# Performance work log

Measured on AMD Instinct MI355X. Metric: run time of the kernel, lower is better.

Reference implementation:

```python
import jax, jax.numpy as jnp
import numpy as np

B, S, E, H = 2, 4096, 768, 12
D = E // H  # head_dim = 64
SCALE = D ** -0.5
NEG = -1e9


def setup_inputs() -> dict:
    key = jax.random.key(0)
    ks = jax.random.split(key, 10)
    init = lambda k, shape: jax.random.normal(k, shape, dtype=jnp.float32) * (shape[-1] ** -0.5)
    x = jax.random.normal(ks[0], (B, S, E), dtype=jnp.float32)
    attention_mask = jnp.zeros((B, 1, S, S), dtype=jnp.float32)
    # additive causal mask: 0 on/below diagonal, -1e9 above
    causal = jnp.where(jnp.tril(jnp.ones((S, S), dtype=bool)), 0.0, NEG).astype(jnp.float32)
    causal_attention_mask = causal[None, None]
    return {
        "x": x,
        "attention_mask": attention_mask,
        "causal_attention_mask": causal_attention_mask,
        "Wq": init(ks[1], (E, E)), "bq": jnp.zeros((E,), jnp.float32),
        "Wk": init(ks[2], (E, E)), "bk": jnp.zeros((E,), jnp.float32),
        "Wv": init(ks[3], (E, E)), "bv": jnp.zeros((E,), jnp.float32),
        "Wo": init(ks[4], (E, E)), "bo": jnp.zeros((E,), jnp.float32),
    }


def _split_heads(t):
    # [B,S,E] -> [B,H,S,D]
    return t.reshape(B, S, H, D).transpose(0, 2, 1, 3)


def reference(x, attention_mask, causal_attention_mask, Wq, bq, Wk, bk, Wv, bv, Wo, bo):
    q = _split_heads(x @ Wq.T + bq)
    k = _split_heads(x @ Wk.T + bk)
    v = _split_heads(x @ Wv.T + bv)
    mask = attention_mask + causal_attention_mask  # [B,1,S,S]
    scores = jnp.einsum("bhqd,bhkd->bhqk", q, k) * SCALE + mask
    probs = jax.nn.softmax(scores.astype(jnp.float32), axis=-1).astype(q.dtype)
    out = jnp.einsum("bhqk,bhkd->bhqd", probs, v)
    out = out.transpose(0, 2, 1, 3).reshape(B, S, E)
    return out @ Wo.T + bo
```

## Files before the change

### kernel.cpp

```cpp
#include <hip/hip_runtime.h>
#include <hip/hip_bf16.h>
#include <stdint.h>

#define B_ 2
#define S_ 4096
#define E_ 768
#define H_ 12
#define D_ 64
#define M_TOT (B_*S_)
#define NQKV (3*E_)

typedef __attribute__((ext_vector_type(8)))  short bf16x8;
typedef __attribute__((ext_vector_type(4)))  float f32x4;
typedef __attribute__((ext_vector_type(16))) float f32x16;
typedef unsigned short u16;
typedef unsigned int   u32;

__device__ __forceinline__ u16 f2bf(float f) {
  __hip_bfloat16 h = __float2bfloat16(f);
  return *reinterpret_cast<u16*>(&h);
}

__device__ __forceinline__ u32 cvtpk(float lo, float hi) {
  u32 r;
  asm("v_cvt_pk_bf16_f32 %0, %1, %2" : "=v"(r) : "v"(lo), "v"(hi));
  return r;
}

#define GLDS(gp, lp) __builtin_amdgcn_global_load_lds( \
    (const __attribute__((address_space(1))) void*)(gp), \
    (__attribute__((address_space(3))) void*)(lp), 16, 0, 0)


__global__ void k_cast_x(const float* __restrict__ x, u16* __restrict__ xb) {
  int i = blockIdx.x * blockDim.x + threadIdx.x;
  float4 v = reinterpret_cast<const float4*>(x)[i];
  ushort4 o;
  o.x = f2bf(v.x); o.y = f2bf(v.y); o.z = f2bf(v.z); o.w = f2bf(v.w);
  reinterpret_cast<ushort4*>(xb)[i] = o;
}

#define QSCALE 0.1803368801111573f

__global__ void k_pack_wqkv(const float* __restrict__ Wq, const float* __restrict__ Wk,
                            const float* __restrict__ Wv, const float* __restrict__ bq,
                            const float* __restrict__ bk, const float* __restrict__ bv,
                            u16* __restrict__ wqkv, float* __restrict__ bqkv) {
  int i = blockIdx.x * blockDim.x + threadIdx.x;
  int base = i * 4;
  int n = base / E_;
  int k = base % E_;
  const float* src; float sc;
  if (n < E_)        { src = Wq + (size_t)n*E_ + k;          sc = QSCALE; }
  else if (n < 2*E_) { src = Wk + (size_t)(n-E_)*E_ + k;     sc = 1.f; }
  else               { src = Wv + (size_t)(n-2*E_)*E_ + k;   sc = 1.f; }
  float4 v = *reinterpret_cast<const float4*>(src);
  ushort4 o;
  o.x = f2bf(v.x*sc); o.y = f2bf(v.y*sc); o.z = f2bf(v.z*sc); o.w = f2bf(v.w*sc);
  reinterpret_cast<ushort4*>(wqkv)[i] = o;
  if (i < NQKV) {
    float b = (i < E_) ? bq[i]*QSCALE : (i < 2*E_) ? bk[i-E_] : bv[i-2*E_];
    bqkv[i] = b;
  }
}

__global__ void k_cast_wo(const float* __restrict__ Wo, u16* __restrict__ wo) {
  int i = blockIdx.x * blockDim.x + threadIdx.x;
  float4 v = reinterpret_cast<const float4*>(Wo)[i];
  ushort4 o;
  o.x = f2bf(v.x); o.y = f2bf(v.y); o.z = f2bf(v.z); o.w = f2bf(v.w);
  reinterpret_cast<ushort4*>(wo)[i] = o;
}


template<int MODE>
__global__ __launch_bounds__(256)
void k_gemm(const u16* __restrict__ A, const u16* __restrict__ W,
            const float* __restrict__ bias,
            u16* __restrict__ dq, u16* __restrict__ dk, u16* __restrict__ dv,
            float* __restrict__ fout)
{
  __shared__ u16 As[128*64];
  __shared__ u16 Ws[128*64];
  const int tid  = threadIdx.x;
  const int lane = tid & 63, wave = tid >> 6;
  const int m0 = blockIdx.x * 128;
  const int n0 = blockIdx.y * 128;
  const int g  = lane >> 4, cc = lane & 15;
  const int wr = (wave >> 1) * 64, wc = (wave & 1) * 64;
  const int srow = lane >> 3;
  const int scol = (lane & 7) * 8;

  f32x4 acc[4][4];
  #pragma unroll
  for (int m = 0; m < 4; ++m)
    #pragma unroll
    for (int n = 0; n < 4; ++n) acc[m][n] = (f32x4){0.f,0.f,0.f,0.f};

  for (int k0 = 0; k0 < E_; k0 += 64) {
    __syncthreads();
    #pragma unroll
    for (int i = 0; i < 4; ++i) {
      const int r0 = (i*4 + wave) * 8;
      GLDS(A + (size_t)(m0 + r0 + srow)*E_ + k0 + scol, As + r0*64);
      GLDS(W + (size_t)(n0 + r0 + srow)*E_ + k0 + scol, Ws + r0*64);
    }
    __syncthreads();
    #pragma unroll
    for (int kk = 0; kk < 64; kk += 32) {
      bf16x8 af[4], bfr[4];
      #pragma unroll
      for (int m = 0; m < 4; ++m)
        af[m] = *reinterpret_cast<const bf16x8*>(As + (wr + m*16 + cc)*64 + kk + g*8);
      #pragma unroll
      for (int n = 0; n < 4; ++n)
        bfr[n] = *reinterpret_cast<const bf16x8*>(Ws + (wc + n*16 + cc)*64 + kk + g*8);
      #pragma unroll
      for (int m = 0; m < 4; ++m)
        #pragma unroll
        for (int n = 0; n < 4; ++n)
          acc[m][n] = __builtin_amdgcn_mfma_f32_16x16x32_bf16(af[m], bfr[n], acc[m][n], 0, 0, 0);
    }
  }

  #pragma unroll
  for (int n = 0; n < 4; ++n) {
    const int colg = n0 + wc + n*16 + cc;
    const float bb = bias[colg];
    if (MODE == 0) {
      const int which = colg / E_;
      const int nn = colg % E_;
      const int h = nn >> 6, d = nn & 63;
      #pragma unroll
      for (int m = 0; m < 4; ++m)
        #pragma unroll
        for (int j = 0; j < 4; ++j) {
          const int row = m0 + wr + m*16 + g*4 + j;
          const int b = row >> 12, s = row & (S_-1);
          const u16 val = f2bf(acc[m][n][j] + bb);
          if (which == 0)       dq[(((size_t)b*H_ + h)*S_ + s)*D_ + d] = val;
          else if (which == 1)  dk[(((size_t)b*H_ + h)*S_ + s)*D_ + d] = val;
          else                  dv[(((size_t)b*H_ + h)*D_ + d)*S_ + s] = val;
        }
    } else {
      #pragma unroll
      for (int m = 0; m < 4; ++m)
        #pragma unroll
        for (int j = 0; j < 4; ++j) {
          const int row = m0 + wr + m*16 + g*4 + j;
          fout[(size_t)row*E_ + colg] = acc[m][n][j] + bb;
        }
    }
  }
}


__global__ __launch_bounds__(256, 3)
void k_attn(const u16* __restrict__ Qb, const u16* __restrict__ Kb,
            const u16* __restrict__ Vtg, u16* __restrict__ AO)
{
  __shared__ u16 Ks[2][32*128];
  __shared__ u16 Vs[2][32*128];
  const int tid = threadIdx.x, lane = tid & 63, w = tid >> 6;

  const int L  = blockIdx.x;
  const int kk = L >> 8;
  const int j  = L & 255;
  const int x  = j & 7;
  const int c  = j >> 3;
  const int bh = x*3 + kk;
  const int u  = c >> 1;
  int qt;
  if (kk == 0)      qt = c;
  else if (kk == 1) qt = (c & 1) ? ((u < 15) ? 14 - u : 15) : 31 - u;
  else              qt = (c & 1) ? ((u < 15) ? 31 - u : 0)  : 16 - u;

  const int q0 = qt * 128;
  const int ntiles = 2*qt + 2;

  const size_t kbase = (size_t)bh * S_ * D_;
  const size_t vbase = (size_t)bh * D_ * S_;
  const int hi = lane >> 5, l31 = lane & 31;
  const int swz = (lane & 15) << 4;
  const int qg = q0 + w*32 + l31;

  int stA[2], stB[2];
  #pragma unroll
  for (int i = 0; i < 2; ++i) {
    const int jj = 2*w + i;
    const int row = jj*4 + (lane >> 4);
    const int gb = ((lane & 15) * 16) ^ ((row & 15) << 4);
    stA[i] = row + 32*(gb >> 7);
    stB[i] = (gb & 127) >> 1;
  }

  bf16x8 qf[4];
  #pragma unroll
  for (int ds = 0; ds < 4; ++ds)
    qf[ds] = *reinterpret_cast<const bf16x8*>(Qb + kbase + (size_t)qg*D_ + ds*16 + hi*8);

  float m_run = -INFINITY, l_run = 0.f;
  f32x16 o0, o1;
  #pragma unroll
  for (int r = 0; r < 16; ++r) { o0[r] = 0.f; o1[r] = 0.f; }

#define STAGE(buf, kv0_) do { \
    _Pragma("unroll") \
    for (int i = 0; i < 2; ++i) { \
      GLDS(Kb  + kbase + (size_t)((kv0_) + stA[i])*D_ + stB[i], &Ks[buf][(2*w+i)*512]); \
      GLDS(Vtg + vbase + (size_t)stA[i]*S_ + (kv0_) + stB[i],   &Vs[buf][(2*w+i)*512]); \
    } } while(0)

  int cur = 0;
  STAGE(0, 0);

  for (int t = 0; t < ntiles; ++t) {
    const int kv0 = t * 64;
    asm volatile("s_waitcnt vmcnt(0)" ::: "memory");
    __builtin_amdgcn_s_barrier();
    asm volatile("" ::: "memory");
    if (t + 1 < ntiles) STAGE(cur ^ 1, (t+1)*64);

    const u16* bK = Ks[cur];
    const u16* bV = Vs[cur];

    f32x16 s0, s1;
    #pragma unroll
    for (int r = 0; r < 16; ++r) { s0[r] = 0.f; s1[r] = 0.f; }
    __builtin_amdgcn_s_setprio(1);
    #pragma unroll
    for (int ds = 0; ds < 4; ++ds) {
      const int off = ((32*ds + 16*hi) ^ swz) >> 1;
      bf16x8 a0 = *reinterpret_cast<const bf16x8*>(bK + l31*128 + off);
      bf16x8 a1 = *reinterpret_cast<const bf16x8*>(bK + l31*128 + (off ^ 64));
      s0 = __builtin_amdgcn_mfma_f32_32x32x16_bf16(a0, qf[ds], s0, 0, 0, 0);
      s1 = __builtin_amdgcn_mfma_f32_32x32x16_bf16(a1, qf[ds], s1, 0, 0, 0);
    }
    __builtin_amdgcn_s_setprio(0);

    if (t >= ntiles - 2) {
      #pragma unroll
      for (int r = 0; r < 16; ++r) {
        const int kvl = kv0 + (r&3) + 8*(r>>2) + 4*hi;
        s0[r] = (kvl      > qg) ? -1e30f : s0[r];
        s1[r] = (kvl + 32 > qg) ? -1e30f : s1[r];
      }
    }

    float m4[8];
    #pragma unroll
    for (int i = 0; i < 4; ++i)
      m4[i] = fmaxf(fmaxf(s0[4*i], s0[4*i+1]), fmaxf(s0[4*i+2], s0[4*i+3]));
    #pragma unroll
    for (int i = 0; i < 4; ++i)
      m4[4+i] = fmaxf(fmaxf(s1[4*i], s1[4*i+1]), fmaxf(s1[4*i+2], s1[4*i+3]));
    float mx = fmaxf(fmaxf(fmaxf(m4[0], m4[1]), fmaxf(m4[2], m4[3])),
                     fmaxf(fmaxf(m4[4], m4[5]), fmaxf(m4[6], m4[7])));
    mx = fmaxf(mx, __shfl_xor(mx, 32));

    if (!__all(mx <= m_run + 8.0f)) {
      const float mnew  = fmaxf(m_run, mx);
      const float alpha = exp2f(m_run - mnew);
      m_run = mnew;
      l_run *= alpha;
      #pragma unroll
      for (int r = 0; r < 16; ++r) { o0[r] *= alpha; o1[r] *= alpha; }
    }

    #pragma unroll
    for (int r = 0; r < 16; ++r) s0[r] = exp2f(s0[r] - m_run);
    #pragma unroll
    for (int r = 0; r < 16; ++r) s1[r] = exp2f(s1[r] - m_run);
    float t4[8];
    #pragma unroll
    for (int i = 0; i < 4; ++i)
      t4[i] = (s0[4*i] + s0[4*i+1]) + (s0[4*i+2] + s0[4*i+3]);
    #pragma unroll
    for (int i = 0; i < 4; ++i)
      t4[4+i] = (s1[4*i] + s1[4*i+1]) + (s1[4*i+2] + s1[4*i+3]);
    float sum = ((t4[0]+t4[1]) + (t4[2]+t4[3])) + ((t4[4]+t4[5]) + (t4[6]+t4[7]));
    sum += __shfl_xor(sum, 32);
    l_run += sum;

    u32 c16[16];
    #pragma unroll
    for (int i = 0; i < 8; ++i) {
      c16[i]   = cvtpk(s0[2*i], s0[2*i+1]);
      c16[8+i] = cvtpk(s1[2*i], s1[2*i+1]);
    }

    #pragma unroll
    for (int ks = 0; ks < 4; ++ks) {
      const int cb = (ks>>1)*8 + (ks&1)*4;
      u32 x0 = c16[cb],   y0 = c16[cb+2];
      u32 x1 = c16[cb+1], y1 = c16[cb+3];
      asm volatile("v_permlane32_swap_b32 %0, %1" : "+v"(x0), "+v"(y0));
      asm volatile("v_permlane32_swap_b32 %0, %1" : "+v"(x1), "+v"(y1));
      union { u32 u[4]; bf16x8 v; } pf;
      pf.u[0] = x0; pf.u[1] = x1; pf.u[2] = y0; pf.u[3] = y1;
      const int voff = ((32*ks + 16*hi) ^ swz) >> 1;
      bf16x8 v0 = *reinterpret_cast<const bf16x8*>(bV + l31*128 + voff);
      bf16x8 v1 = *reinterpret_cast<const bf16x8*>(bV + l31*128 + (voff ^ 64));
      __builtin_amdgcn_s_setprio(1);
      o0 = __builtin_amdgcn_mfma_f32_32x32x16_bf16(v0, pf.v, o0, 0, 0, 0);
      o1 = __builtin_amdgcn_mfma_f32_32x32x16_bf16(v1, pf.v, o1, 0, 0, 0);
      __builtin_amdgcn_s_setprio(0);
    }

    asm volatile("" ::: "memory");
    __builtin_amdgcn_s_barrier();
    cur ^= 1;
  }
#undef STAGE

  const int b = bh / H_, h = bh % H_;
  const float inv = 1.0f / l_run;
  u16* dst = AO + ((size_t)b*S_ + qg)*E_ + h*64;
  #pragma unroll
  for (int aa = 0; aa < 4; ++aa) {
    ushort4 wv;
    wv.x = f2bf(o0[4*aa+0]*inv); wv.y = f2bf(o0[4*aa+1]*inv);
    wv.z = f2bf(o0[4*aa+2]*inv); wv.w = f2bf(o0[4*aa+3]*inv);
    *reinterpret_cast<ushort4*>(dst + aa*8 + hi*4) = wv;
  }
  #pragma unroll
  for (int aa = 0; aa < 4; ++aa) {
    ushort4 wv;
    wv.x = f2bf(o1[4*aa+0]*inv); wv.y = f2bf(o1[4*aa+1]*inv);
    wv.z = f2bf(o1[4*aa+2]*inv); wv.w = f2bf(o1[4*aa+3]*inv);
    *reinterpret_cast<ushort4*>(dst + 32 + aa*8 + hi*4) = wv;
  }
}


extern "C" void kernel_launch(void* const* d_in, const int* in_sizes, int n_in,
                              void* d_out, int out_size, void* d_ws, size_t ws_size,
                              hipStream_t stream) {
  const float* x  = (const float*)d_in[0];
  const float* Wq = (const float*)d_in[3];
  const float* bq = (const float*)d_in[4];
  const float* Wk = (const float*)d_in[5];
  const float* bk = (const float*)d_in[6];
  const float* Wv = (const float*)d_in[7];
  const float* bv = (const float*)d_in[8];
  const float* Wo = (const float*)d_in[9];
  const float* bo = (const float*)d_in[10];
  float* out = (float*)d_out;

  const size_t SZ_X   = (size_t)M_TOT * E_ * 2;
  const size_t SZ_WQKV= (size_t)NQKV * E_ * 2;
  const size_t SZ_WO  = (size_t)E_ * E_ * 2;
  const size_t SZ_B   = (size_t)NQKV * 4;
  char* w = (char*)d_ws;
  u16*   xb   = (u16*)(w);
  u16*   wqkv = (u16*)(w + SZ_X);
  u16*   wob  = (u16*)(w + SZ_X + SZ_WQKV);
  float* bqkv = (float*)(w + SZ_X + SZ_WQKV + SZ_WO);
  char*  w2   = w + SZ_X + SZ_WQKV + SZ_WO + SZ_B;
  u16* Qb = (u16*)(w2);
  u16* Kb = (u16*)(w2 + SZ_X);
  u16* Vb = (u16*)(w2 + 2*SZ_X);
  u16* AO = (u16*)(w2 + 3*SZ_X);

  k_cast_x  <<<6144, 256, 0, stream>>>(x, xb);
  k_pack_wqkv<<<1728, 256, 0, stream>>>(Wq, Wk, Wv, bq, bk, bv, wqkv, bqkv);
  k_cast_wo <<<576,  256, 0, stream>>>(Wo, wob);

  dim3 gq(64, 18);
  k_gemm<0><<<gq, 256, 0, stream>>>(xb, wqkv, bqkv, Qb, Kb, Vb, nullptr);

  k_attn<<<768, 256, 0, stream>>>(Qb, Kb, Vb, AO);

  dim3 go(64, 6);
  k_gemm<1><<<go, 256, 0, stream>>>(AO, wob, bo, nullptr, nullptr, nullptr, out);
}
```

Before: 233.6 us.

## Split long causal attention rows across two blocks and merge with combine kernel

The attention kernel now splits the KV range of the longer query tiles (qt>=16) into two partial blocks. Each block writes unnormalized bf16 partial outputs plus its running max and sum, and a new k_comb kernel merges the two halves. This is meant to balance work across CUs and shorten the critical path. The block-to-work schedule is rebuilt for 1152 blocks and occupancy is raised to 5 per CU. Diagonal tiles are processed first so the running max starts from real values, the max reduction uses v_max3, and rescaling is folded into the score init. The costs are an extra launch, the partial-result traffic through a reused workspace buffer, and one more bf16 rounding of the partials.

New measurement: 285.6 us. 1.22x slower.

```diff
diff --git a/kernel.cpp b/kernel.cpp
--- a/kernel.cpp
+++ b/kernel.cpp
@@ -21,15 +21,27 @@
   return *reinterpret_cast<u16*>(&h);
 }
 
+__device__ __forceinline__ float bf2f(u16 u) {
+  union { u32 i; float f; } v; v.i = ((u32)u) << 16; return v.f;
+}
+
 __device__ __forceinline__ u32 cvtpk(float lo, float hi) {
   u32 r;
   asm("v_cvt_pk_bf16_f32 %0, %1, %2" : "=v"(r) : "v"(lo), "v"(hi));
   return r;
 }
 
+__device__ __forceinline__ float max3f(float a, float b, float c) {
+  float d;
+  asm("v_max3_f32 %0, %1, %2, %3" : "=v"(d) : "v"(a), "v"(b), "v"(c));
+  return d;
+}
+
 #define GLDS(gp, lp) __builtin_amdgcn_global_load_lds( \
     (const __attribute__((address_space(1))) void*)(gp), \
     (__attribute__((address_space(3))) void*)(lp), 16, 0, 0)
+
+#define QSCALE 0.1803368801111573f
 
 
 __global__ void k_cast_x(const float* __restrict__ x, u16* __restrict__ xb) {
@@ -39,8 +51,6 @@
   o.x = f2bf(v.x); o.y = f2bf(v.y); o.z = f2bf(v.z); o.w = f2bf(v.w);
   reinterpret_cast<ushort4*>(xb)[i] = o;
 }
-
-#define QSCALE 0.1803368801111573f
 
 __global__ void k_pack_wqkv(const float* __restrict__ Wq, const float* __restrict__ Wk,
                             const float* __restrict__ Wv, const float* __restrict__ bq,
@@ -51,9 +61,9 @@
   int n = base / E_;
   int k = base % E_;
   const float* src; float sc;
-  if (n < E_)        { src = Wq + (size_t)n*E_ + k;          sc = QSCALE; }
-  else if (n < 2*E_) { src = Wk + (size_t)(n-E_)*E_ + k;     sc = 1.f; }
-  else               { src = Wv + (size_t)(n-2*E_)*E_ + k;   sc = 1.f; }
+  if (n < E_)        { src = Wq + (size_t)n*E_ + k;        sc = QSCALE; }
+  else if (n < 2*E_) { src = Wk + (size_t)(n-E_)*E_ + k;   sc = 1.f; }
+  else               { src = Wv + (size_t)(n-2*E_)*E_ + k; sc = 1.f; }
   float4 v = *reinterpret_cast<const float4*>(src);
   ushort4 o;
   o.x = f2bf(v.x*sc); o.y = f2bf(v.y*sc); o.z = f2bf(v.z*sc); o.w = f2bf(v.w*sc);
@@ -155,34 +165,44 @@
 }
 
 
-__global__ __launch_bounds__(256, 3)
+__global__ __launch_bounds__(256, 5)
 void k_attn(const u16* __restrict__ Qb, const u16* __restrict__ Kb,
-            const u16* __restrict__ Vtg, u16* __restrict__ AO)
+            const u16* __restrict__ Vtg, u16* __restrict__ AO,
+            u16* __restrict__ PO, float2* __restrict__ PML)
 {
   __shared__ u16 Ks[2][32*128];
   __shared__ u16 Vs[2][32*128];
   const int tid = threadIdx.x, lane = tid & 63, w = tid >> 6;
 
-  const int L  = blockIdx.x;
-  const int kk = L >> 8;
-  const int j  = L & 255;
-  const int x  = j & 7;
-  const int c  = j >> 3;
-  const int bh = x*3 + kk;
-  const int u  = c >> 1;
-  int qt;
-  if (kk == 0)      qt = c;
-  else if (kk == 1) qt = (c & 1) ? ((u < 15) ? 14 - u : 15) : 31 - u;
-  else              qt = (c & 1) ? ((u < 15) ? 31 - u : 0)  : 16 - u;
-
+  const int L    = blockIdx.x;
+  const int slot = L >> 8;
+  const int cu   = L & 255;
+  const int x    = cu & 7;
+  const int c    = cu >> 3;
+  int r;
+  if (slot < 4) r = slot*32 + ((slot & 1) ? (31 - c) : c);
+  else          r = 128 + c;
+  int head, qt, mode;
+  if (r < 120) {
+    const int g_ = r / 15, o = r % 15;
+    if (o < 9) {
+      if (o < 3) { head = o; qt = 15 - g_; mode = 0; }
+      else { const int hh = o - 3; head = hh >> 1; mode = 1 + (hh & 1); qt = 31 - 2*g_; }
+    } else { const int hh = o - 9; head = hh >> 1; mode = 1 + (hh & 1); qt = 30 - 2*g_; }
+  } else {
+    const int rr = r - 120; qt = 7 - rr/3; head = rr % 3; mode = 0;
+  }
+  const int bh = x*3 + head;
   const int q0 = qt * 128;
-  const int ntiles = 2*qt + 2;
+  const int nt = (mode == 0) ? (2*qt + 2) : (qt + 1);
 
   const size_t kbase = (size_t)bh * S_ * D_;
   const size_t vbase = (size_t)bh * D_ * S_;
   const int hi = lane >> 5, l31 = lane & 31;
   const int swz = (lane & 15) << 4;
   const int qg = q0 + w*32 + l31;
+
+  #define KVT(it_) ((mode == 1) ? (it_) : ((it_) == 0 ? 2*qt : ((it_) == 1 ? 2*qt+1 : ((mode == 0) ? (it_) - 2 : qt + (it_) - 1))))
 
   int stA[2], stB[2];
   #pragma unroll
@@ -199,10 +219,10 @@
   for (int ds = 0; ds < 4; ++ds)
     qf[ds] = *reinterpret_cast<const bf16x8*>(Qb + kbase + (size_t)qg*D_ + ds*16 + hi*8);
 
-  float m_run = -INFINITY, l_run = 0.f;
+  float m_run = 0.f, l_run = 0.f;
   f32x16 o0, o1;
   #pragma unroll
-  for (int r = 0; r < 16; ++r) { o0[r] = 0.f; o1[r] = 0.f; }
+  for (int r2 = 0; r2 < 16; ++r2) { o0[r2] = 0.f; o1[r2] = 0.f; }
 
 #define STAGE(buf, kv0_) do { \
     _Pragma("unroll") \
@@ -212,21 +232,22 @@
     } } while(0)
 
   int cur = 0;
-  STAGE(0, 0);
-
-  for (int t = 0; t < ntiles; ++t) {
-    const int kv0 = t * 64;
+  STAGE(0, KVT(0)*64);
+
+  for (int it = 0; it < nt; ++it) {
     asm volatile("s_waitcnt vmcnt(0)" ::: "memory");
     __builtin_amdgcn_s_barrier();
     asm volatile("" ::: "memory");
-    if (t + 1 < ntiles) STAGE(cur ^ 1, (t+1)*64);
-
+    if (it + 1 < nt) STAGE(cur ^ 1, KVT(it+1)*64);
+
+    const int kv0 = KVT(it) * 64;
     const u16* bK = Ks[cur];
     const u16* bV = Vs[cur];
 
+    const float minit = (it == 0) ? 0.f : -m_run;
     f32x16 s0, s1;
     #pragma unroll
-    for (int r = 0; r < 16; ++r) { s0[r] = 0.f; s1[r] = 0.f; }
+    for (int r2 = 0; r2 < 16; ++r2) { s0[r2] = minit; s1[r2] = minit; }
     __builtin_amdgcn_s_setprio(1);
     #pragma unroll
     for (int ds = 0; ds < 4; ++ds) {
@@ -238,39 +259,52 @@
     }
     __builtin_amdgcn_s_setprio(0);
 
-    if (t >= ntiles - 2) {
-      #pragma unroll
-      for (int r = 0; r < 16; ++r) {
-        const int kvl = kv0 + (r&3) + 8*(r>>2) + 4*hi;
-        s0[r] = (kvl      > qg) ? -1e30f : s0[r];
-        s1[r] = (kvl + 32 > qg) ? -1e30f : s1[r];
+    if (mode != 1 && it <= 1) {
+      #pragma unroll
+      for (int r2 = 0; r2 < 16; ++r2) {
+        const int kvl = kv0 + (r2&3) + 8*(r2>>2) + 4*hi;
+        s0[r2] = (kvl      > qg) ? -1e30f : s0[r2];
+        s1[r2] = (kvl + 32 > qg) ? -1e30f : s1[r2];
       }
     }
 
-    float m4[8];
-    #pragma unroll
-    for (int i = 0; i < 4; ++i)
-      m4[i] = fmaxf(fmaxf(s0[4*i], s0[4*i+1]), fmaxf(s0[4*i+2], s0[4*i+3]));
-    #pragma unroll
-    for (int i = 0; i < 4; ++i)
-      m4[4+i] = fmaxf(fmaxf(s1[4*i], s1[4*i+1]), fmaxf(s1[4*i+2], s1[4*i+3]));
-    float mx = fmaxf(fmaxf(fmaxf(m4[0], m4[1]), fmaxf(m4[2], m4[3])),
-                     fmaxf(fmaxf(m4[4], m4[5]), fmaxf(m4[6], m4[7])));
+    float a0_ = max3f(s0[0],  s0[1],  s0[2]);
+    float a1_ = max3f(s0[3],  s0[4],  s0[5]);
+    float a2_ = max3f(s0[6],  s0[7],  s0[8]);
+    float a3_ = max3f(s0[9],  s0[10], s0[11]);
+    float a4_ = max3f(s0[12], s0[13], s0[14]);
+    float a5_ = max3f(s1[0],  s1[1],  s1[2]);
+    float a6_ = max3f(s1[3],  s1[4],  s1[5]);
+    float a7_ = max3f(s1[6],  s1[7],  s1[8]);
+    float a8_ = max3f(s1[9],  s1[10], s1[11]);
+    float a9_ = max3f(s1[12], s1[13], s1[14]);
+    float b0_ = max3f(a0_, a1_, a2_);
+    float b1_ = max3f(a3_, a4_, s0[15]);
+    float b2_ = max3f(a5_, a6_, a7_);
+    float b3_ = max3f(a8_, a9_, s1[15]);
+    float mx  = max3f(b0_, b1_, fmaxf(b2_, b3_));
     mx = fmaxf(mx, __shfl_xor(mx, 32));
 
-    if (!__all(mx <= m_run + 8.0f)) {
-      const float mnew  = fmaxf(m_run, mx);
-      const float alpha = exp2f(m_run - mnew);
-      m_run = mnew;
+    if (it == 0) {
+      m_run = mx;
+      #pragma unroll
+      for (int r2 = 0; r2 < 16; ++r2) { s0[r2] -= mx; s1[r2] -= mx; }
+    } else if (!__all(mx <= 24.0f)) {
+      const float mxc   = fmaxf(mx, 0.f);
+      const float alpha = exp2f(-mxc);
+      m_run += mxc;
       l_run *= alpha;
       #pragma unroll
-      for (int r = 0; r < 16; ++r) { o0[r] *= alpha; o1[r] *= alpha; }
-    }
-
-    #pragma unroll
-    for (int r = 0; r < 16; ++r) s0[r] = exp2f(s0[r] - m_run);
-    #pragma unroll
-    for (int r = 0; r < 16; ++r) s1[r] = exp2f(s1[r] - m_run);
+      for (int r2 = 0; r2 < 16; ++r2) {
+        o0[r2] *= alpha; o1[r2] *= alpha;
+        s0[r2] -= mxc;   s1[r2] -= mxc;
+      }
+    }
+    #pragma unroll
+    for (int r2 = 0; r2 < 16; ++r2) s0[r2] = exp2f(s0[r2]);
+    #pragma unroll
+    for (int r2 = 0; r2 < 16; ++r2) s1[r2] = exp2f(s1[r2]);
+
     float t4[8];
     #pragma unroll
     for (int i = 0; i < 4; ++i)
@@ -312,23 +346,87 @@
     cur ^= 1;
   }
 #undef STAGE
-
+#undef KVT
+
+  if (mode == 0) {
+    const int b = bh / H_, h = bh % H_;
+    const float inv = 1.0f / l_run;
+    u16* dst = AO + ((size_t)b*S_ + qg)*E_ + h*64;
+    #pragma unroll
+    for (int aa = 0; aa < 4; ++aa) {
+      ushort4 wv;
+      wv.x = f2bf(o0[4*aa+0]*inv); wv.y = f2bf(o0[4*aa+1]*inv);
+      wv.z = f2bf(o0[4*aa+2]*inv); wv.w = f2bf(o0[4*aa+3]*inv);
+      *reinterpret_cast<ushort4*>(dst + aa*8 + hi*4) = wv;
+    }
+    #pragma unroll
+    for (int aa = 0; aa < 4; ++aa) {
+      ushort4 wv;
+      wv.x = f2bf(o1[4*aa+0]*inv); wv.y = f2bf(o1[4*aa+1]*inv);
+      wv.z = f2bf(o1[4*aa+2]*inv); wv.w = f2bf(o1[4*aa+3]*inv);
+      *reinterpret_cast<ushort4*>(dst + 32 + aa*8 + hi*4) = wv;
+    }
+  } else {
+    const int qslot = (bh*16 + (qt-16))*2 + (mode - 1);
+    const int rowt = w*32 + l31;
+    u16* po = PO + (size_t)qslot*(128*64) + rowt*64;
+    #pragma unroll
+    for (int aa = 0; aa < 4; ++aa) {
+      ushort4 wv;
+      wv.x = f2bf(o0[4*aa+0]); wv.y = f2bf(o0[4*aa+1]);
+      wv.z = f2bf(o0[4*aa+2]); wv.w = f2bf(o0[4*aa+3]);
+      *reinterpret_cast<ushort4*>(po + aa*8 + hi*4) = wv;
+    }
+    #pragma unroll
+    for (int aa = 0; aa < 4; ++aa) {
+      ushort4 wv;
+      wv.x = f2bf(o1[4*aa+0]); wv.y = f2bf(o1[4*aa+1]);
+      wv.z = f2bf(o1[4*aa+2]); wv.w = f2bf(o1[4*aa+3]);
+      *reinterpret_cast<ushort4*>(po + 32 + aa*8 + hi*4) = wv;
+    }
+    if (hi == 0) PML[qslot*128 + rowt] = make_float2(m_run, l_run);
+  }
+}
+
+
+__global__ __launch_bounds__(256)
+void k_comb(const u16* __restrict__ PO, const float2* __restrict__ PML,
+            u16* __restrict__ AO)
+{
+  const int bid = blockIdx.x;
+  const int bh = bid >> 4, qi = bid & 15, q = 16 + qi;
+  const int t = threadIdx.x;
+  const int r = t >> 1, half = t & 1;
+  const int s0 = (bh*16 + qi)*2, s1 = s0 + 1;
+  const float2 ml0 = PML[s0*128 + r];
+  const float2 ml1 = PML[s1*128 + r];
+  const float mstar = fmaxf(ml0.x, ml1.x);
+  const float w0 = exp2f(ml0.x - mstar);
+  const float w1 = exp2f(ml1.x - mstar);
+  const float inv = 1.0f / (ml0.y*w0 + ml1.y*w1);
+  const float a0 = w0 * inv, a1 = w1 * inv;
+  const u16* p0 = PO + (size_t)s0*(128*64) + r*64 + half*32;
+  const u16* p1 = PO + (size_t)s1*(128*64) + r*64 + half*32;
   const int b = bh / H_, h = bh % H_;
-  const float inv = 1.0f / l_run;
-  u16* dst = AO + ((size_t)b*S_ + qg)*E_ + h*64;
-  #pragma unroll
-  for (int aa = 0; aa < 4; ++aa) {
-    ushort4 wv;
-    wv.x = f2bf(o0[4*aa+0]*inv); wv.y = f2bf(o0[4*aa+1]*inv);
-    wv.z = f2bf(o0[4*aa+2]*inv); wv.w = f2bf(o0[4*aa+3]*inv);
-    *reinterpret_cast<ushort4*>(dst + aa*8 + hi*4) = wv;
-  }
-  #pragma unroll
-  for (int aa = 0; aa < 4; ++aa) {
-    ushort4 wv;
-    wv.x = f2bf(o1[4*aa+0]*inv); wv.y = f2bf(o1[4*aa+1]*inv);
-    wv.z = f2bf(o1[4*aa+2]*inv); wv.w = f2bf(o1[4*aa+3]*inv);
-    *reinterpret_cast<ushort4*>(dst + 32 + aa*8 + hi*4) = wv;
+  const int row = q*128 + r;
+  u16* dst = AO + ((size_t)b*S_ + row)*E_ + h*64 + half*32;
+  #pragma unroll
+  for (int i = 0; i < 4; ++i) {
+    bf16x8 v0 = *reinterpret_cast<const bf16x8*>(p0 + i*8);
+    bf16x8 v1 = *reinterpret_cast<const bf16x8*>(p1 + i*8);
+    ushort4 lo, hi4;
+    float f0 = bf2f(((const u16*)&v0)[0])*a0 + bf2f(((const u16*)&v1)[0])*a1;
+    float f1 = bf2f(((const u16*)&v0)[1])*a0 + bf2f(((const u16*)&v1)[1])*a1;
+    float f2 = bf2f(((const u16*)&v0)[2])*a0 + bf2f(((const u16*)&v1)[2])*a1;
+    float f3 = bf2f(((const u16*)&v0)[3])*a0 + bf2f(((const u16*)&v1)[3])*a1;
+    lo.x = f2bf(f0); lo.y = f2bf(f1); lo.z = f2bf(f2); lo.w = f2bf(f3);
+    float f4 = bf2f(((const u16*)&v0)[4])*a0 + bf2f(((const u16*)&v1)[4])*a1;
+    float f5 = bf2f(((const u16*)&v0)[5])*a0 + bf2f(((const u16*)&v1)[5])*a1;
+    float f6 = bf2f(((const u16*)&v0)[6])*a0 + bf2f(((const u16*)&v1)[6])*a1;
+    float f7 = bf2f(((const u16*)&v0)[7])*a0 + bf2f(((const u16*)&v1)[7])*a1;
+    hi4.x = f2bf(f4); hi4.y = f2bf(f5); hi4.z = f2bf(f6); hi4.w = f2bf(f7);
+    *reinterpret_cast<ushort4*>(dst + i*8)     = lo;
+    *reinterpret_cast<ushort4*>(dst + i*8 + 4) = hi4;
   }
 }
 
@@ -361,6 +459,8 @@
   u16* Kb = (u16*)(w2 + SZ_X);
   u16* Vb = (u16*)(w2 + 2*SZ_X);
   u16* AO = (u16*)(w2 + 3*SZ_X);
+  u16* PO = xb;
+  float2* PML = (float2*)(w2 + 4*SZ_X);
 
   k_cast_x  <<<6144, 256, 0, stream>>>(x, xb);
   k_pack_wqkv<<<1728, 256, 0, stream>>>(Wq, Wk, Wv, bq, bk, bv, wqkv, bqkv);
@@ -369,7 +469,8 @@
   dim3 gq(64, 18);
   k_gemm<0><<<gq, 256, 0, stream>>>(xb, wqkv, bqkv, Qb, Kb, Vb, nullptr);
 
-  k_attn<<<768, 256, 0, stream>>>(Qb, Kb, Vb, AO);
+  k_attn<<<1152, 256, 0, stream>>>(Qb, Kb, Vb, AO, PO, PML);
+  k_comb<<<384, 256, 0, stream>>>(PO, PML, AO);
 
   dim3 go(64, 6);
   k_gemm<1><<<go, 256, 0, stream>>>(AO, wob, bo, nullptr, nullptr, nullptr, out);
```
